# Kernel optimization log

Hardware: AMD Instinct MI355X
Metric: run time of the kernel (lower is better)

The kernel has to match this reference:

```python
import jax, jax.numpy as jnp
import numpy as np

EMB = 512
NUM_HEAD = 8
HEAD_DIM = EMB // NUM_HEAD  # 64
B, S = 16, 2048


def setup_inputs() -> dict:
    key = jax.random.key(0)
    k1, k2, k3, k4 = jax.random.split(key, 4)
    x1 = jax.random.normal(k1, (B, S, EMB), dtype=jnp.float32)
    # causal mask: 1 where attention allowed, 0 elsewhere (masked_fill where mask==0)
    mask = jnp.tril(jnp.ones((S, S), dtype=jnp.int32))
    scale = 1.0 / np.sqrt(EMB)
    Wq = jax.random.normal(k2, (EMB, HEAD_DIM), dtype=jnp.float32) * scale
    Wk = jax.random.normal(k3, (EMB, HEAD_DIM), dtype=jnp.float32) * scale
    Wv = jax.random.normal(k4, (EMB, HEAD_DIM), dtype=jnp.float32) * scale
    return {"x1": x1, "mask": mask, "Wq": Wq, "Wk": Wk, "Wv": Wv}


def reference(x1, mask, Wq, Wk, Wv):
    # q,k,v: [B,S,H]
    q = jnp.einsum('bse,eh->bsh', x1, Wq)
    k = jnp.einsum('bse,eh->bsh', x1, Wk)
    v = jnp.einsum('bse,eh->bsh', x1, Wv)
    # scores: [B,S,S]
    scaled_qk = jnp.einsum('bqh,bkh->bqk', q, k) / jnp.sqrt(jnp.float32(HEAD_DIM))
    scaled_qk = jnp.where(mask == 0, -jnp.inf, scaled_qk)
    attn = jax.nn.softmax(scaled_qk, axis=-1)
    return jnp.einsum('bqk,bkh->bqh', attn, v)
```

## Files before the change

### kernel.cpp

```cpp
#include <hip/hip_runtime.h>
#include <hip/hip_bf16.h>

typedef __attribute__((ext_vector_type(8))) short bf16x8;
typedef __attribute__((ext_vector_type(4))) float f32x4;
typedef __attribute__((ext_vector_type(4))) unsigned short u16x4;

#define MFMA16(a, b, c) __builtin_amdgcn_mfma_f32_16x16x32_bf16(a, b, c, 0, 0, 0)

#define QSCALE 0.18033688011112042f

#define GLDS16(gp, lp)                                                         \
    __builtin_amdgcn_global_load_lds(                                          \
        (const __attribute__((address_space(1))) void*)(gp),                   \
        (__attribute__((address_space(3))) void*)(lp), 16, 0, 0)

__device__ __forceinline__ short nbf(float f) {
    __hip_bfloat16 h = __float2bfloat16(f);
    return *(short*)&h;
}
__device__ __forceinline__ unsigned short nbfu(float f) {
    __hip_bfloat16 h = __float2bfloat16(f);
    return *(unsigned short*)&h;
}

__global__ void wt_kernel(const float* __restrict__ Wq, const float* __restrict__ Wk,
                          const float* __restrict__ Wv, unsigned short* __restrict__ Wt) {
    const int h = blockIdx.x;
    const int mat = blockIdx.y;
    const int e = threadIdx.x;
    const float* W = (mat == 0) ? Wq : ((mat == 1) ? Wk : Wv);
    Wt[(mat * 64 + h) * 512 + e] = nbfu(W[e * 64 + h]);
}

__global__ __launch_bounds__(512, 1) void qkv_proj(
    const float* __restrict__ x1, const unsigned short* __restrict__ Wt,
    unsigned short* __restrict__ Q, unsigned short* __restrict__ Kf,
    unsigned short* __restrict__ Vf)
{
    __shared__ char alds[2][16384];
    __shared__ char blds[2][12288];

    const int tid = threadIdx.x;
    const int W = tid >> 6, lane = tid & 63;
    const int c = lane & 15, g = lane >> 4;
    const int tokB = blockIdx.x * 128;

    const char* x1b = (const char*)x1;
    const char* Wtb = (const char*)Wt;

    const int tA0 = tid >> 3,           qA0 = (tid & 7) ^ (tA0 & 7);
    const int tA1 = (tid + 512) >> 3,   qA1 = (tid & 7) ^ (tA1 & 7);
    const size_t aoff0 = (size_t)(tokB + tA0) * 2048 + qA0 * 16;
    const size_t aoff1 = (size_t)(tokB + tA1) * 2048 + qA1 * 16;

    auto bsrc = [&](int j) -> size_t {
        const int n = j >> 6, c2 = (j >> 2) & 15, g2 = j & 3;
        return (size_t)((n >> 2) * 64 + (n & 3) * 16 + c2) * 1024 + g2 * 16;
    };
    const size_t boff0 = bsrc(tid), boff1 = bsrc(tid + 512);

    f32x4 acc[12];
#pragma unroll
    for (int n = 0; n < 12; ++n) acc[n] = (f32x4)0.f;

    GLDS16(x1b + aoff0, &alds[0][tid * 16]);
    GLDS16(x1b + aoff1, &alds[0][8192 + tid * 16]);
    GLDS16(Wtb + boff0, &blds[0][tid * 16]);
    if (tid < 256) GLDS16(Wtb + boff1, &blds[0][8192 + tid * 16]);

    const int arow = (W * 16 + c) * 128;
    const int aq0 = (((2 * g) ^ (c & 7)) * 16);
    const int aq1 = (((2 * g + 1) ^ (c & 7)) * 16);
    const int brd = (c * 4 + g) * 16;

    int buf = 0;
    for (int ks = 0; ks < 16; ++ks) {
        asm volatile("s_waitcnt vmcnt(0)\n\ts_barrier" ::: "memory");

        if (ks < 15) {
            const size_t ka = (size_t)(ks + 1) * 128;
            const size_t kb = (size_t)(ks + 1) * 64;
            char* ab = &alds[buf ^ 1][0];
            char* bb = &blds[buf ^ 1][0];
            GLDS16(x1b + aoff0 + ka, ab + tid * 16);
            GLDS16(x1b + aoff1 + ka, ab + 8192 + tid * 16);
            GLDS16(Wtb + boff0 + kb, bb + tid * 16);
            if (tid < 256) GLDS16(Wtb + boff1 + kb, bb + 8192 + tid * 16);
        }

        const char* ab = &alds[buf][0];
        const char* bb = &blds[buf][0];
        f32x4 a0 = *(const f32x4*)(ab + arow + aq0);
        f32x4 a1 = *(const f32x4*)(ab + arow + aq1);
        bf16x8 af;
        af[0] = nbf(a0[0]); af[1] = nbf(a0[1]); af[2] = nbf(a0[2]); af[3] = nbf(a0[3]);
        af[4] = nbf(a1[0]); af[5] = nbf(a1[1]); af[6] = nbf(a1[2]); af[7] = nbf(a1[3]);
#pragma unroll
        for (int n = 0; n < 12; ++n) {
            bf16x8 bf = *(const bf16x8*)(bb + n * 1024 + brd);
            acc[n] = MFMA16(af, bf, acc[n]);
        }
        buf ^= 1;
    }

    const int tok0 = tokB + W * 16;
    const int bb2 = tokB >> 11;
    const int ht = ((tokB & 2047) >> 6) + (W >> 2);

#pragma unroll
    for (int n = 0; n < 4; ++n)
#pragma unroll
        for (int r = 0; r < 4; ++r)
            Q[(size_t)(tok0 + g * 4 + r) * 64 + n * 16 + c] = nbfu(acc[n][r] * QSCALE);

    {
        unsigned short* kf = Kf + (size_t)bb2 * 131072 + (size_t)ht * 4096;
#pragma unroll
        for (int n = 0; n < 4; ++n) {
            const int gf = (n & 1) * 2 + (c >> 3);
            const size_t base = (size_t)(n >> 1) * 2048 + (W & 3) * 512 + (c & 7);
#pragma unroll
            for (int r = 0; r < 4; ++r)
                kf[base + (size_t)(gf * 16 + g * 4 + r) * 8] = nbfu(acc[4 + n][r]);
        }
    }

    {
        unsigned short* vf = Vf + (size_t)bb2 * 131072 + (size_t)ht * 4096;
        const int sub = (W & 3) >> 1;
        const int gf = (W & 1) * 2 + (g >> 1);
        const int jb = (g & 1) * 4;
#pragma unroll
        for (int n = 0; n < 4; ++n) {
            u16x4 pv;
#pragma unroll
            for (int r = 0; r < 4; ++r) pv[r] = nbfu(acc[8 + n][r]);
            *(u16x4*)(vf + (size_t)sub * 2048 + n * 512 + (gf * 16 + c) * 8 + jb) = pv;
        }
    }
}

__global__ __launch_bounds__(512, 2) void flash_attn(
    const unsigned short* __restrict__ Q, const unsigned short* __restrict__ Kf,
    const unsigned short* __restrict__ Vf, float* __restrict__ out)
{
    __shared__ char kv[2][65536];
    __shared__ char p_lds[32768];

    const int tid = threadIdx.x;
    const int W = tid >> 6;
    const int st = W >> 2;
    const int w = W & 3;
    const int lane = tid & 63;
    const int c = lane & 15, g = lane >> 4;

    const int id = blockIdx.x;
    const int b = 2 * (id & 7) + ((id >> 3) & 1);
    const int qt = 31 - (id >> 4);
    const int n2 = (qt >> 1) + 1;
    const int J = (n2 + 1) >> 1;
    const int qr0c = qt * 64 + w * 16 + c;
    const size_t qrow_g = ((size_t)b << 11) + qt * 64 + w * 16;

    bf16x8 qf0 = *(const bf16x8*)(Q + (qrow_g + c) * 64 + g * 8);
    bf16x8 qf1 = *(const bf16x8*)(Q + (qrow_g + c) * 64 + 32 + g * 8);

    const char* Kfb = (const char*)(Kf + (size_t)b * 131072);
    const char* Vfb = (const char*)(Vf + (size_t)b * 131072);

    const int off0 = tid * 16, off1 = (tid + 512) * 16;

    float m = -1e30f, l = 0.f;
    f32x4 acc[4];
#pragma unroll
    for (int n = 0; n < 4; ++n) acc[n] = (f32x4)0.f;

    auto STAGE = [&](int p, char* d) {
        const size_t o0 = (size_t)(2 * p) * 16384;
        const size_t o1 = o0 + 16384;
        GLDS16(Kfb + o0 + off0, d + off0);
        GLDS16(Kfb + o0 + off1, d + off1);
        GLDS16(Vfb + o0 + off0, d + 16384 + off0);
        GLDS16(Vfb + o0 + off1, d + 16384 + off1);
        GLDS16(Kfb + o1 + off0, d + 32768 + off0);
        GLDS16(Kfb + o1 + off1, d + 32768 + off1);
        GLDS16(Vfb + o1 + off0, d + 49152 + off0);
        GLDS16(Vfb + o1 + off1, d + 49152 + off1);
    };

    STAGE(0, &kv[0][0]);

    for (int j = 0; j < J; ++j) {
        asm volatile("s_waitcnt vmcnt(0)\n\ts_barrier" ::: "memory");

        if (j + 1 < J) STAGE(j + 1, &kv[(j & 1) ^ 1][0]);

        const int t = 2 * j + st;
        if (t < n2) {
            const char* kb = &kv[j & 1][st * 32768];
            const char* vb = kb + 16384;

            bf16x8 kfA[8], kfB[8];
#pragma unroll
            for (int h = 0; h < 2; ++h)
#pragma unroll
                for (int n = 0; n < 4; ++n) {
                    kfA[h * 4 + n] = *(const bf16x8*)(kb + h * 8192 + n * 1024 + lane * 16);
                    kfB[h * 4 + n] = *(const bf16x8*)(kb + h * 8192 + 4096 + n * 1024 + lane * 16);
                }
            f32x4 s[8];
#pragma unroll
            for (int i = 0; i < 8; ++i) s[i] = (f32x4)0.f;
            __builtin_amdgcn_s_setprio(1);
#pragma unroll
            for (int i = 0; i < 8; ++i) {
                s[i] = MFMA16(kfA[i], qf0, s[i]);
                s[i] = MFMA16(kfB[i], qf1, s[i]);
            }
            __builtin_amdgcn_s_setprio(0);

            if (t == n2 - 1) {
#pragma unroll
                for (int h = 0; h < 2; ++h)
#pragma unroll
                    for (int n = 0; n < 4; ++n) {
                        const int key0 = t * 128 + h * 64 + n * 16 + g * 4;
#pragma unroll
                        for (int r = 0; r < 4; ++r)
                            if (key0 + r > qr0c) s[h * 4 + n][r] = -1e30f;
                    }
            }

            float tm = -1e30f;
#pragma unroll
            for (int i = 0; i < 8; ++i)
                tm = fmaxf(tm, fmaxf(fmaxf(s[i][0], s[i][1]), fmaxf(s[i][2], s[i][3])));

            if (__any(tm > m + 8.f)) {
                float gm = tm;
                gm = fmaxf(gm, __shfl_xor(gm, 16, 64));
                gm = fmaxf(gm, __shfl_xor(gm, 32, 64));
                const float mn = fmaxf(m, gm);
                const float alpha = exp2f(m - mn);
                m = mn;
                l *= alpha;
                float al[4];
#pragma unroll
                for (int r = 0; r < 4; ++r) al[r] = __shfl(alpha, g * 4 + r, 16);
#pragma unroll
                for (int n = 0; n < 4; ++n)
#pragma unroll
                    for (int r = 0; r < 4; ++r) acc[n][r] *= al[r];
            }

            char* pw = &p_lds[W * 4096 + ((g >> 1) * 16 + c) * 16 + (g & 1) * 8];
#pragma unroll
            for (int h = 0; h < 2; ++h)
#pragma unroll
                for (int n = 0; n < 4; ++n) {
                    const int i = h * 4 + n;
                    float p0 = exp2f(s[i][0] - m);
                    float p1 = exp2f(s[i][1] - m);
                    float p2 = exp2f(s[i][2] - m);
                    float p3 = exp2f(s[i][3] - m);
                    l += (p0 + p1) + (p2 + p3);
                    u16x4 pk;
                    pk[0] = nbfu(p0); pk[1] = nbfu(p1); pk[2] = nbfu(p2); pk[3] = nbfu(p3);
                    *(u16x4*)(pw + (h * 2 + (n >> 1)) * 1024 + (n & 1) * 512) = pk;
                }

            const char* pr = &p_lds[W * 4096 + lane * 16];
            bf16x8 pf[4];
#pragma unroll
            for (int ps = 0; ps < 4; ++ps) pf[ps] = *(const bf16x8*)(pr + ps * 1024);

            __builtin_amdgcn_s_setprio(1);
#pragma unroll
            for (int n = 0; n < 4; ++n)
#pragma unroll
                for (int ps = 0; ps < 4; ++ps) {
                    bf16x8 vf = *(const bf16x8*)(vb + (ps >> 1) * 8192 + (ps & 1) * 4096 + n * 1024 + lane * 16);
                    acc[n] = MFMA16(pf[ps], vf, acc[n]);
                }
            __builtin_amdgcn_s_setprio(0);
        }
    }

    __syncthreads();
    float* accb = (float*)&kv[0][0];
    float* mb = (float*)&kv[0][16384];
    float* lb = (float*)&kv[0][16384 + 256];

    if (st == 1) {
        l += __shfl_xor(l, 16, 64);
        l += __shfl_xor(l, 32, 64);
        if (g == 0) { mb[w * 16 + c] = m; lb[w * 16 + c] = l; }
#pragma unroll
        for (int n = 0; n < 4; ++n)
#pragma unroll
            for (int r = 0; r < 4; ++r)
                accb[w * 1024 + (g * 4 + r) * 64 + n * 16 + c] = acc[n][r];
    }
    __syncthreads();

    if (st == 0) {
        l += __shfl_xor(l, 16, 64);
        l += __shfl_xor(l, 32, 64);
        const float m1c = mb[w * 16 + c];
        const float l1c = lb[w * 16 + c];
        const float mF = fmaxf(m, m1c);
        const float a0 = exp2f(m - mF);
        const float a1 = (m1c > -1e29f) ? exp2f(m1c - mF) : 0.f;
        const float inv = 1.f / (l * a0 + l1c * a1);
        const float s0 = a0 * inv, s1 = a1 * inv;
        float s0r[4], s1r[4];
#pragma unroll
        for (int r = 0; r < 4; ++r) {
            s0r[r] = __shfl(s0, g * 4 + r, 16);
            s1r[r] = __shfl(s1, g * 4 + r, 16);
        }
#pragma unroll
        for (int n = 0; n < 4; ++n)
#pragma unroll
            for (int r = 0; r < 4; ++r) {
                const float a1v = accb[w * 1024 + (g * 4 + r) * 64 + n * 16 + c];
                out[(qrow_g + g * 4 + r) * 64 + n * 16 + c] = acc[n][r] * s0r[r] + a1v * s1r[r];
            }
    }
}

extern "C" void kernel_launch(void* const* d_in, const int* in_sizes, int n_in,
                              void* d_out, int out_size, void* d_ws, size_t ws_size,
                              hipStream_t stream) {
    const float* x1 = (const float*)d_in[0];
    const float* Wq = (const float*)d_in[2];
    const float* Wk = (const float*)d_in[3];
    const float* Wv = (const float*)d_in[4];
    float* out = (float*)d_out;

    unsigned short* Wt  = (unsigned short*)d_ws;
    unsigned short* Qw  = (unsigned short*)((char*)d_ws + 196608);
    unsigned short* Kfw = (unsigned short*)((char*)d_ws + 196608 + 4194304);
    unsigned short* Vfw = (unsigned short*)((char*)d_ws + 196608 + 2 * 4194304);

    wt_kernel<<<dim3(64, 3), 512, 0, stream>>>(Wq, Wk, Wv, Wt);
    qkv_proj<<<256, 512, 0, stream>>>(x1, Wt, Qw, Kfw, Vfw);
    flash_attn<<<512, 512, 0, stream>>>(Qw, Kfw, Vfw, out);
}
```

Before: 57.93 us.

## Drop LDS double-buffered K/V staging; read K/V fragments directly from global

Removes the 128KB double-buffered LDS staging of K/V tiles and its per-iteration block barriers. Each wave group now reads K and V fragments straight from global memory and interleaves the loads with the MFMAs. This cuts LDS use enough to raise launch bounds to 4 blocks per CU for more occupancy and latency hiding. The cost is that K/V reuse across the four waves of a group now relies on L1/L2 caching, with more global load traffic and exposed load latency.

```diff
diff --git a/kernel.cpp b/kernel.cpp
--- a/kernel.cpp
+++ b/kernel.cpp
@@ -140,12 +140,12 @@
     }
 }
 
-__global__ __launch_bounds__(512, 2) void flash_attn(
+__global__ __launch_bounds__(512, 4) void flash_attn(
     const unsigned short* __restrict__ Q, const unsigned short* __restrict__ Kf,
     const unsigned short* __restrict__ Vf, float* __restrict__ out)
 {
-    __shared__ char kv[2][65536];
     __shared__ char p_lds[32768];
+    __shared__ float mb[4][16], lb[4][16];
 
     const int tid = threadIdx.x;
     const int W = tid >> 6;
@@ -158,7 +158,6 @@
     const int b = 2 * (id & 7) + ((id >> 3) & 1);
     const int qt = 31 - (id >> 4);
     const int n2 = (qt >> 1) + 1;
-    const int J = (n2 + 1) >> 1;
     const int qr0c = qt * 64 + w * 16 + c;
     const size_t qrow_g = ((size_t)b << 11) + qt * 64 + w * 16;
 
@@ -168,133 +167,108 @@
     const char* Kfb = (const char*)(Kf + (size_t)b * 131072);
     const char* Vfb = (const char*)(Vf + (size_t)b * 131072);
 
-    const int off0 = tid * 16, off1 = (tid + 512) * 16;
-
     float m = -1e30f, l = 0.f;
     f32x4 acc[4];
 #pragma unroll
     for (int n = 0; n < 4; ++n) acc[n] = (f32x4)0.f;
 
-    auto STAGE = [&](int p, char* d) {
-        const size_t o0 = (size_t)(2 * p) * 16384;
-        const size_t o1 = o0 + 16384;
-        GLDS16(Kfb + o0 + off0, d + off0);
-        GLDS16(Kfb + o0 + off1, d + off1);
-        GLDS16(Vfb + o0 + off0, d + 16384 + off0);
-        GLDS16(Vfb + o0 + off1, d + 16384 + off1);
-        GLDS16(Kfb + o1 + off0, d + 32768 + off0);
-        GLDS16(Kfb + o1 + off1, d + 32768 + off1);
-        GLDS16(Vfb + o1 + off0, d + 49152 + off0);
-        GLDS16(Vfb + o1 + off1, d + 49152 + off1);
-    };
-
-    STAGE(0, &kv[0][0]);
-
-    for (int j = 0; j < J; ++j) {
-        asm volatile("s_waitcnt vmcnt(0)\n\ts_barrier" ::: "memory");
-
-        if (j + 1 < J) STAGE(j + 1, &kv[(j & 1) ^ 1][0]);
-
-        const int t = 2 * j + st;
-        if (t < n2) {
-            const char* kb = &kv[j & 1][st * 32768];
-            const char* vb = kb + 16384;
-
-            bf16x8 kfA[8], kfB[8];
-#pragma unroll
-            for (int h = 0; h < 2; ++h)
-#pragma unroll
-                for (int n = 0; n < 4; ++n) {
-                    kfA[h * 4 + n] = *(const bf16x8*)(kb + h * 8192 + n * 1024 + lane * 16);
-                    kfB[h * 4 + n] = *(const bf16x8*)(kb + h * 8192 + 4096 + n * 1024 + lane * 16);
-                }
-            f32x4 s[8];
-#pragma unroll
-            for (int i = 0; i < 8; ++i) s[i] = (f32x4)0.f;
+    for (int t = st; t < n2; t += 2) {
+        const char* kt = Kfb + (size_t)t * 16384;
+        const char* vt = Vfb + (size_t)t * 16384;
+
+        f32x4 s[8];
+#pragma unroll
+        for (int i = 0; i < 8; ++i) s[i] = (f32x4)0.f;
+#pragma unroll
+        for (int h = 0; h < 2; ++h) {
+            bf16x8 ka[4], kb2[4];
+#pragma unroll
+            for (int n = 0; n < 4; ++n) {
+                ka[n]  = *(const bf16x8*)(kt + h * 8192 + n * 1024 + lane * 16);
+                kb2[n] = *(const bf16x8*)(kt + h * 8192 + 4096 + n * 1024 + lane * 16);
+            }
             __builtin_amdgcn_s_setprio(1);
 #pragma unroll
-            for (int i = 0; i < 8; ++i) {
-                s[i] = MFMA16(kfA[i], qf0, s[i]);
-                s[i] = MFMA16(kfB[i], qf1, s[i]);
+            for (int n = 0; n < 4; ++n) {
+                s[h * 4 + n] = MFMA16(ka[n], qf0, s[h * 4 + n]);
+                s[h * 4 + n] = MFMA16(kb2[n], qf1, s[h * 4 + n]);
             }
             __builtin_amdgcn_s_setprio(0);
-
-            if (t == n2 - 1) {
-#pragma unroll
-                for (int h = 0; h < 2; ++h)
-#pragma unroll
-                    for (int n = 0; n < 4; ++n) {
-                        const int key0 = t * 128 + h * 64 + n * 16 + g * 4;
-#pragma unroll
-                        for (int r = 0; r < 4; ++r)
-                            if (key0 + r > qr0c) s[h * 4 + n][r] = -1e30f;
-                    }
+        }
+
+        if (t == n2 - 1) {
+#pragma unroll
+            for (int h = 0; h < 2; ++h)
+#pragma unroll
+                for (int n = 0; n < 4; ++n) {
+                    const int key0 = t * 128 + h * 64 + n * 16 + g * 4;
+#pragma unroll
+                    for (int r = 0; r < 4; ++r)
+                        if (key0 + r > qr0c) s[h * 4 + n][r] = -1e30f;
+                }
+        }
+
+        float tm = -1e30f;
+#pragma unroll
+        for (int i = 0; i < 8; ++i)
+            tm = fmaxf(tm, fmaxf(fmaxf(s[i][0], s[i][1]), fmaxf(s[i][2], s[i][3])));
+
+        if (__any(tm > m + 8.f)) {
+            float gm = tm;
+            gm = fmaxf(gm, __shfl_xor(gm, 16, 64));
+            gm = fmaxf(gm, __shfl_xor(gm, 32, 64));
+            const float mn = fmaxf(m, gm);
+            const float alpha = exp2f(m - mn);
+            m = mn;
+            l *= alpha;
+            float al[4];
+#pragma unroll
+            for (int r = 0; r < 4; ++r) al[r] = __shfl(alpha, g * 4 + r, 16);
+#pragma unroll
+            for (int n = 0; n < 4; ++n)
+#pragma unroll
+                for (int r = 0; r < 4; ++r) acc[n][r] *= al[r];
+        }
+
+        char* pw = &p_lds[W * 4096 + ((g >> 1) * 16 + c) * 16 + (g & 1) * 8];
+#pragma unroll
+        for (int h = 0; h < 2; ++h)
+#pragma unroll
+            for (int n = 0; n < 4; ++n) {
+                const int i = h * 4 + n;
+                float p0 = exp2f(s[i][0] - m);
+                float p1 = exp2f(s[i][1] - m);
+                float p2 = exp2f(s[i][2] - m);
+                float p3 = exp2f(s[i][3] - m);
+                l += (p0 + p1) + (p2 + p3);
+                u16x4 pk;
+                pk[0] = nbfu(p0); pk[1] = nbfu(p1); pk[2] = nbfu(p2); pk[3] = nbfu(p3);
+                *(u16x4*)(pw + (h * 2 + (n >> 1)) * 1024 + (n & 1) * 512) = pk;
             }
 
-            float tm = -1e30f;
-#pragma unroll
-            for (int i = 0; i < 8; ++i)
-                tm = fmaxf(tm, fmaxf(fmaxf(s[i][0], s[i][1]), fmaxf(s[i][2], s[i][3])));
-
-            if (__any(tm > m + 8.f)) {
-                float gm = tm;
-                gm = fmaxf(gm, __shfl_xor(gm, 16, 64));
-                gm = fmaxf(gm, __shfl_xor(gm, 32, 64));
-                const float mn = fmaxf(m, gm);
-                const float alpha = exp2f(m - mn);
-                m = mn;
-                l *= alpha;
-                float al[4];
-#pragma unroll
-                for (int r = 0; r < 4; ++r) al[r] = __shfl(alpha, g * 4 + r, 16);
-#pragma unroll
-                for (int n = 0; n < 4; ++n)
-#pragma unroll
-                    for (int r = 0; r < 4; ++r) acc[n][r] *= al[r];
-            }
-
-            char* pw = &p_lds[W * 4096 + ((g >> 1) * 16 + c) * 16 + (g & 1) * 8];
-#pragma unroll
-            for (int h = 0; h < 2; ++h)
-#pragma unroll
-                for (int n = 0; n < 4; ++n) {
-                    const int i = h * 4 + n;
-                    float p0 = exp2f(s[i][0] - m);
-                    float p1 = exp2f(s[i][1] - m);
-                    float p2 = exp2f(s[i][2] - m);
-                    float p3 = exp2f(s[i][3] - m);
-                    l += (p0 + p1) + (p2 + p3);
-                    u16x4 pk;
-                    pk[0] = nbfu(p0); pk[1] = nbfu(p1); pk[2] = nbfu(p2); pk[3] = nbfu(p3);
-                    *(u16x4*)(pw + (h * 2 + (n >> 1)) * 1024 + (n & 1) * 512) = pk;
-                }
-
-            const char* pr = &p_lds[W * 4096 + lane * 16];
-            bf16x8 pf[4];
-#pragma unroll
-            for (int ps = 0; ps < 4; ++ps) pf[ps] = *(const bf16x8*)(pr + ps * 1024);
-
+        const char* pr = &p_lds[W * 4096 + lane * 16];
+#pragma unroll
+        for (int ps = 0; ps < 4; ++ps) {
+            bf16x8 pf = *(const bf16x8*)(pr + ps * 1024);
+            bf16x8 vf[4];
+#pragma unroll
+            for (int n = 0; n < 4; ++n)
+                vf[n] = *(const bf16x8*)(vt + (ps >> 1) * 8192 + (ps & 1) * 4096 + n * 1024 + lane * 16);
             __builtin_amdgcn_s_setprio(1);
 #pragma unroll
             for (int n = 0; n < 4; ++n)
-#pragma unroll
-                for (int ps = 0; ps < 4; ++ps) {
-                    bf16x8 vf = *(const bf16x8*)(vb + (ps >> 1) * 8192 + (ps & 1) * 4096 + n * 1024 + lane * 16);
-                    acc[n] = MFMA16(pf[ps], vf, acc[n]);
-                }
+                acc[n] = MFMA16(pf, vf[n], acc[n]);
             __builtin_amdgcn_s_setprio(0);
         }
     }
 
     __syncthreads();
-    float* accb = (float*)&kv[0][0];
-    float* mb = (float*)&kv[0][16384];
-    float* lb = (float*)&kv[0][16384 + 256];
+    float* accb = (float*)&p_lds[0];
 
     if (st == 1) {
         l += __shfl_xor(l, 16, 64);
         l += __shfl_xor(l, 32, 64);
-        if (g == 0) { mb[w * 16 + c] = m; lb[w * 16 + c] = l; }
+        if (g == 0) { mb[w][c] = m; lb[w][c] = l; }
 #pragma unroll
         for (int n = 0; n < 4; ++n)
 #pragma unroll
@@ -306,8 +280,8 @@
     if (st == 0) {
         l += __shfl_xor(l, 16, 64);
         l += __shfl_xor(l, 32, 64);
-        const float m1c = mb[w * 16 + c];
-        const float l1c = lb[w * 16 + c];
+        const float m1c = mb[w][c];
+        const float l1c = lb[w][c];
         const float mF = fmaxf(m, m1c);
         const float a0 = exp2f(m - mF);
         const float a1 = (m1c > -1e29f) ? exp2f(m1c - mF) : 0.f;
```

Result: no change. 58.25 us (+0.6%).
